# Kernel tuning notes

Measured on AMD Instinct MI355X. Metric: run time of the kernel, lower is better.

Reference implementation:

```python
import jax, jax.numpy as jnp
import numpy as np

N, K, DIM = 65536, 32, 64


def setup_inputs() -> dict:
    key = jax.random.key(0)
    k1, k2, k3, k4 = jax.random.split(key, 4)
    x = jax.random.normal(k1, (N, DIM), jnp.float32)
    log_pi = jax.random.normal(k2, (K, 1), jnp.float32)
    mu = jax.random.normal(k3, (K, DIM), jnp.float32)
    log_sigma_ = jax.random.normal(k4, (K, DIM, DIM), jnp.float32) / 100.0
    return {"x": x, "log_pi": log_pi, "mu": mu, "log_sigma_": log_sigma_}


def reference(x, log_pi, mu, log_sigma_):
    k, d = mu.shape
    # Faithful to torch: softmax over the size-1 last axis of (K,1) -> all ones.
    pi = jax.nn.softmax(log_pi, axis=-1)  # (K, 1)
    # scale_tril construction: strict lower triangle kept, diagonal -> exp(diag) + 1e-3
    diag = jnp.exp(jnp.diagonal(log_sigma_, axis1=-2, axis2=-1)) + 1e-3  # (K, d)
    L = jnp.tril(log_sigma_, -1) + jnp.eye(d, dtype=x.dtype) * diag[:, None, :]  # (K, d, d)
    # batched MVN log_prob via triangular solve
    diff = x[:, None, :] - mu[None, :, :]            # (N, K, d)
    b = jnp.transpose(diff, (1, 2, 0))               # (K, d, N)
    z = jax.scipy.linalg.solve_triangular(L, b, lower=True)  # (K, d, N)
    maha = jnp.sum(z * z, axis=1)                    # (K, N)
    logdet = jnp.sum(jnp.log(diag), axis=-1)         # (K,)
    logp = -0.5 * (maha + d * jnp.log(2.0 * jnp.pi)) - logdet[:, None]  # (K, N)
    p = jnp.exp(logp).T                              # (N, K)
    return jnp.log(jnp.matmul(p, pi).squeeze())      # (N,)
```

## Files before the change

kernel.cpp:

```cpp
#include <hip/hip_runtime.h>

#define KK 32
#define DD 64
#define NB 65536
#define PAD 68
#define FRAGS 6
#define SLOT (FRAGS * 64)
#define MREF 103.0f
#define L2E 1.4426950408889634f

typedef __attribute__((ext_vector_type(8))) short bf16x8;
typedef __attribute__((ext_vector_type(4))) float f32x4;
typedef __attribute__((ext_vector_type(16))) float f32x16;

__device__ inline short f2bf(float f) {
  uint32_t u = __builtin_bit_cast(uint32_t, f);
  uint32_t r = (u + 0x7fffu + ((u >> 16) & 1u)) >> 16;
  return (short)(r & 0xffffu);
}
__device__ inline uint4 pack8(const short* v) {
  uint4 u;
  u.x = (uint32_t)(unsigned short)v[0] | ((uint32_t)(unsigned short)v[1] << 16);
  u.y = (uint32_t)(unsigned short)v[2] | ((uint32_t)(unsigned short)v[3] << 16);
  u.z = (uint32_t)(unsigned short)v[4] | ((uint32_t)(unsigned short)v[5] << 16);
  u.w = (uint32_t)(unsigned short)v[6] | ((uint32_t)(unsigned short)v[7] << 16);
  return u;
}

__device__ __forceinline__ void gl_lds16(const uint4* g, uint4* l) {
  __builtin_amdgcn_global_load_lds(
      (__attribute__((address_space(1))) void*)g,
      (__attribute__((address_space(3))) void*)l, 16, 0, 0);
}

__global__ __launch_bounds__(256) void md_prep(const float* __restrict__ ls,
                                               const float* __restrict__ mu,
                                               uint4* __restrict__ Bp,
                                               float* __restrict__ Cc,
                                               float* __restrict__ Kcl2) {
  __shared__ float Ls[DD * DD];
  __shared__ float Ys[DD * PAD];
  __shared__ float invdL[DD];
  __shared__ float muL[DD];
  const int k = blockIdx.x, t = threadIdx.x;
  const int j = t >> 2, sub = t & 3;
  const float* __restrict__ lsk = ls + (size_t)k * DD * DD;

#pragma unroll
  for (int it = 0; it < 4; ++it) {
    const int o = (it * 256 + t) * 4;
    *(float4*)&Ls[o] = *(const float4*)&lsk[o];
  }
  if (t < DD) muL[t] = mu[k * DD + t];
  __syncthreads();
  if (t < DD) invdL[t] = 1.0f / (expf(Ls[t * DD + t]) + 1e-3f);
  __syncthreads();

  const float invdj = invdL[j];
  float z[16];
#pragma unroll
  for (int mi = 0; mi < 16; ++mi) z[mi] = 0.f;
#pragma unroll
  for (int i = 0; i < DD; ++i) {
    float p = 0.f;
#pragma unroll
    for (int mi = 0; mi < 16; ++mi) {
      if (4 * mi < i) {
        const int m = 4 * mi + sub;
        p = fmaf(Ls[i * DD + m], (m < i) ? z[mi] : 0.f, p);
      }
    }
    p += __shfl_xor(p, 1, 64);
    p += __shfl_xor(p, 2, 64);
    const float zi = (i == j) ? invdj : -p * invdL[i];
    if (sub == (i & 3)) z[i >> 2] = zi;
  }
#pragma unroll
  for (int mi = 0; mi < 16; ++mi) Ys[(4 * mi + sub) * PAD + j] = z[mi];
  __syncthreads();

  {
    float p = 0.f;
#pragma unroll
    for (int mi = 0; mi < 16; ++mi) {
      const int m = 4 * mi + sub;
      p = fmaf(Ys[j * PAD + m], muL[m], p);
    }
    p += __shfl_xor(p, 1, 64);
    p += __shfl_xor(p, 2, 64);
    if (sub == 0) Cc[k * DD + j] = p;
  }

  if (t < DD) {
    float r = -logf(invdL[t]);
#pragma unroll
    for (int off = 32; off > 0; off >>= 1) r += __shfl_down(r, off, 64);
    if (t == 0)
      Kcl2[k] = (MREF - 0.5f * (64.0f * 1.83787706640934534f) - r) * L2E;
  }

  if (t < DD) {
    const int r32 = t & 31, h = t >> 5;
    uint4* slot = Bp + (size_t)k * SLOT;
#pragma unroll
    for (int it = 0; it < 2; ++it) {
#pragma unroll
      for (int kt = 0; kt < 4; ++kt) {
        if (it == 0 && kt >= 2) continue;
        const int i = it * 32 + r32;
        short hh[8];
#pragma unroll
        for (int jj = 0; jj < 8; ++jj) {
          const int m = kt * 16 + h * 8 + jj;
          const float v = Ys[i * PAD + m] - ((i == m) ? 1.0f : 0.0f);
          hh[jj] = f2bf(v);
        }
        const int fi = (it == 0) ? kt : (2 + kt);
        slot[fi * 64 + t] = pack8(hh);
      }
    }
  }
}

__global__ __launch_bounds__(256, 2) void md_main(const float* __restrict__ x,
                                                  const uint4* __restrict__ Bp,
                                                  const float* __restrict__ Cc,
                                                  const float* __restrict__ Kcl2,
                                                  float* __restrict__ out) {
  __shared__ uint4 lds4[8 * SLOT];
  __shared__ float CcL[KK * DD];
  __shared__ float sOut[2 * 128];
  const int tid = threadIdx.x, lane = tid & 63, w = tid >> 6;
  const int sg = w & 1, kg = w >> 1;
  const int sblk = blockIdx.x;
  const int base = sblk * 128 + sg * 64;
  const int k0 = kg * 16;
  const int c32 = lane & 31, h = lane >> 5;

  bf16x8 Xb[2][4];
#pragma unroll
  for (int st = 0; st < 2; ++st) {
#pragma unroll
    for (int kt = 0; kt < 4; ++kt) {
      const float* src = x + (size_t)(base + st * 32 + c32) * DD + kt * 16 + h * 8;
      const float4 v0 = *(const float4*)src;
      const float4 v1 = *(const float4*)(src + 4);
      const float f[8] = {v0.x, v0.y, v0.z, v0.w, v1.x, v1.y, v1.z, v1.w};
      bf16x8 hb;
#pragma unroll
      for (int jj = 0; jj < 8; ++jj) hb[jj] = f2bf(f[jj]);
      Xb[st][kt] = hb;
    }
  }

  f32x16 xg[2][2];
#pragma unroll
  for (int it = 0; it < 2; ++it)
#pragma unroll
    for (int st = 0; st < 2; ++st)
#pragma unroll
      for (int g = 0; g < 4; ++g) {
        const f32x4 v = *(const f32x4*)&x[(size_t)(base + st * 32 + c32) * DD +
                                          it * 32 + g * 8 + 4 * h];
        xg[it][st][4 * g + 0] = v[0];
        xg[it][st][4 * g + 1] = v[1];
        xg[it][st][4 * g + 2] = v[2];
        xg[it][st][4 * g + 3] = v[3];
      }

#pragma unroll
  for (int it = 0; it < 8; ++it)
    CcL[it * 256 + tid] = Cc[it * 256 + tid];

  {
    const uint4* src = Bp + (size_t)(k0 + sg) * SLOT;
#pragma unroll
    for (int t = 0; t < 6; ++t)
      gl_lds16(src + t * 64 + lane,
               &lds4[((kg * 2 + 0) * 2 + sg) * SLOT + t * 64]);
  }
  __syncthreads();

  float run_s[2] = {0.f, 0.f};

#pragma unroll
  for (int kp = 0; kp < 8; ++kp) {
    const int p = kp & 1;
    if (kp < 7) {
      const uint4* src = Bp + (size_t)(k0 + 2 * (kp + 1) + sg) * SLOT;
#pragma unroll
      for (int t = 0; t < 6; ++t)
        gl_lds16(src + t * 64 + lane,
                 &lds4[((kg * 2 + (1 - p)) * 2 + sg) * SLOT + t * 64]);
    }

#pragma unroll
    for (int c = 0; c < 2; ++c) {
      const int kabs = k0 + 2 * kp + c;
      const float kc = Kcl2[kabs];
      const uint4* buf = &lds4[((kg * 2 + p) * 2 + c) * SLOT];

      f32x4 cv[2][4];
#pragma unroll
      for (int it = 0; it < 2; ++it)
#pragma unroll
        for (int g = 0; g < 4; ++g)
          cv[it][g] = *(const f32x4*)&CcL[kabs * DD + it * 32 + g * 8 + 4 * h];

      const bf16x8 A0 = *(const bf16x8*)&buf[0 * 64 + lane];
      const bf16x8 A1 = *(const bf16x8*)&buf[1 * 64 + lane];
      const bf16x8 A2 = *(const bf16x8*)&buf[2 * 64 + lane];
      const bf16x8 A3 = *(const bf16x8*)&buf[3 * 64 + lane];
      const bf16x8 A4 = *(const bf16x8*)&buf[4 * 64 + lane];
      const bf16x8 A5 = *(const bf16x8*)&buf[5 * 64 + lane];

#pragma unroll
      for (int st = 0; st < 2; ++st) {
        f32x16 acc;
#pragma unroll
        for (int it = 0; it < 2; ++it) {
          f32x16 z;
#pragma unroll
          for (int g = 0; g < 4; ++g) {
#pragma unroll
            for (int r = 0; r < 4; ++r)
              z[4 * g + r] = xg[it][st][4 * g + r] - cv[it][g][r];
          }
          if (it == 0) {
            z = __builtin_amdgcn_mfma_f32_32x32x16_bf16(A0, Xb[st][0], z, 0, 0, 0);
            z = __builtin_amdgcn_mfma_f32_32x32x16_bf16(A1, Xb[st][1], z, 0, 0, 0);
            acc = z * z;
          } else {
            z = __builtin_amdgcn_mfma_f32_32x32x16_bf16(A2, Xb[st][0], z, 0, 0, 0);
            z = __builtin_amdgcn_mfma_f32_32x32x16_bf16(A3, Xb[st][1], z, 0, 0, 0);
            z = __builtin_amdgcn_mfma_f32_32x32x16_bf16(A4, Xb[st][2], z, 0, 0, 0);
            z = __builtin_amdgcn_mfma_f32_32x32x16_bf16(A5, Xb[st][3], z, 0, 0, 0);
            acc += z * z;
          }
        }
        const float t0 = (acc[0] + acc[1]) + (acc[2] + acc[3]);
        const float t1 = (acc[4] + acc[5]) + (acc[6] + acc[7]);
        const float t2 = (acc[8] + acc[9]) + (acc[10] + acc[11]);
        const float t3 = (acc[12] + acc[13]) + (acc[14] + acc[15]);
        float s = (t0 + t1) + (t2 + t3);
        s += __shfl_xor(s, 32, 64);
        const float tt = fmaf(-0.5f * L2E, s, kc);
        run_s[st] += __builtin_amdgcn_exp2f(tt);
      }
    }

    if (kp < 7) __syncthreads();
  }

  if (h == 0) {
#pragma unroll
    for (int st = 0; st < 2; ++st)
      sOut[kg * 128 + sg * 64 + st * 32 + c32] = run_s[st];
  }
  __syncthreads();
  if (tid < 128) {
    const float S = sOut[tid] + sOut[128 + tid];
    out[sblk * 128 + tid] = logf(S) - MREF;
  }
}

extern "C" void kernel_launch(void* const* d_in, const int* in_sizes, int n_in,
                              void* d_out, int out_size, void* d_ws, size_t ws_size,
                              hipStream_t stream) {
  const float* x  = (const float*)d_in[0];
  const float* mu = (const float*)d_in[2];
  const float* ls = (const float*)d_in[3];
  float* out = (float*)d_out;

  char* ws = (char*)d_ws;
  uint4* Bp   = (uint4*)ws;
  float* Cc   = (float*)(ws + (size_t)KK * SLOT * 16);
  float* Kcl2 = Cc + KK * DD;

  md_prep<<<KK, 256, 0, stream>>>(ls, mu, Bp, Cc, Kcl2);
  md_main<<<NB / 128, 256, 0, stream>>>(x, Bp, Cc, Kcl2, out);
}
```

Measured before the change: 99.56 us.

## Load MFMA A-fragments directly from global memory instead of LDS double-buffer

Removes the async global-to-LDS double-buffered staging of per-component B fragments and the per-iteration block barriers. Each wave now reads its bf16 A operands straight from global/L2 for each of its 16 components. This frees LDS (possibly raising occupancy) and removes synchronization, at the cost of exposing global load latency before each MFMA chain, since nothing is prefetched.

Result: no change. 98.33 us (median of 2 runs) (-1.2%).

```diff
diff --git a/kernel.cpp b/kernel.cpp
--- a/kernel.cpp
+++ b/kernel.cpp
@@ -25,12 +25,6 @@
   u.z = (uint32_t)(unsigned short)v[4] | ((uint32_t)(unsigned short)v[5] << 16);
   u.w = (uint32_t)(unsigned short)v[6] | ((uint32_t)(unsigned short)v[7] << 16);
   return u;
-}
-
-__device__ __forceinline__ void gl_lds16(const uint4* g, uint4* l) {
-  __builtin_amdgcn_global_load_lds(
-      (__attribute__((address_space(1))) void*)g,
-      (__attribute__((address_space(3))) void*)l, 16, 0, 0);
 }
 
 __global__ __launch_bounds__(256) void md_prep(const float* __restrict__ ls,
@@ -127,7 +121,6 @@
                                                   const float* __restrict__ Cc,
                                                   const float* __restrict__ Kcl2,
                                                   float* __restrict__ out) {
-  __shared__ uint4 lds4[8 * SLOT];
   __shared__ float CcL[KK * DD];
   __shared__ float sOut[2 * 128];
   const int tid = threadIdx.x, lane = tid & 63, w = tid >> 6;
@@ -171,85 +164,63 @@
 #pragma unroll
   for (int it = 0; it < 8; ++it)
     CcL[it * 256 + tid] = Cc[it * 256 + tid];
-
-  {
-    const uint4* src = Bp + (size_t)(k0 + sg) * SLOT;
-#pragma unroll
-    for (int t = 0; t < 6; ++t)
-      gl_lds16(src + t * 64 + lane,
-               &lds4[((kg * 2 + 0) * 2 + sg) * SLOT + t * 64]);
-  }
   __syncthreads();
 
   float run_s[2] = {0.f, 0.f};
 
 #pragma unroll
-  for (int kp = 0; kp < 8; ++kp) {
-    const int p = kp & 1;
-    if (kp < 7) {
-      const uint4* src = Bp + (size_t)(k0 + 2 * (kp + 1) + sg) * SLOT;
-#pragma unroll
-      for (int t = 0; t < 6; ++t)
-        gl_lds16(src + t * 64 + lane,
-                 &lds4[((kg * 2 + (1 - p)) * 2 + sg) * SLOT + t * 64]);
-    }
-
-#pragma unroll
-    for (int c = 0; c < 2; ++c) {
-      const int kabs = k0 + 2 * kp + c;
-      const float kc = Kcl2[kabs];
-      const uint4* buf = &lds4[((kg * 2 + p) * 2 + c) * SLOT];
-
-      f32x4 cv[2][4];
-#pragma unroll
-      for (int it = 0; it < 2; ++it)
-#pragma unroll
-        for (int g = 0; g < 4; ++g)
-          cv[it][g] = *(const f32x4*)&CcL[kabs * DD + it * 32 + g * 8 + 4 * h];
-
-      const bf16x8 A0 = *(const bf16x8*)&buf[0 * 64 + lane];
-      const bf16x8 A1 = *(const bf16x8*)&buf[1 * 64 + lane];
-      const bf16x8 A2 = *(const bf16x8*)&buf[2 * 64 + lane];
-      const bf16x8 A3 = *(const bf16x8*)&buf[3 * 64 + lane];
-      const bf16x8 A4 = *(const bf16x8*)&buf[4 * 64 + lane];
-      const bf16x8 A5 = *(const bf16x8*)&buf[5 * 64 + lane];
-
-#pragma unroll
-      for (int st = 0; st < 2; ++st) {
-        f32x16 acc;
-#pragma unroll
-        for (int it = 0; it < 2; ++it) {
-          f32x16 z;
-#pragma unroll
-          for (int g = 0; g < 4; ++g) {
-#pragma unroll
-            for (int r = 0; r < 4; ++r)
-              z[4 * g + r] = xg[it][st][4 * g + r] - cv[it][g][r];
-          }
-          if (it == 0) {
-            z = __builtin_amdgcn_mfma_f32_32x32x16_bf16(A0, Xb[st][0], z, 0, 0, 0);
-            z = __builtin_amdgcn_mfma_f32_32x32x16_bf16(A1, Xb[st][1], z, 0, 0, 0);
-            acc = z * z;
-          } else {
-            z = __builtin_amdgcn_mfma_f32_32x32x16_bf16(A2, Xb[st][0], z, 0, 0, 0);
-            z = __builtin_amdgcn_mfma_f32_32x32x16_bf16(A3, Xb[st][1], z, 0, 0, 0);
-            z = __builtin_amdgcn_mfma_f32_32x32x16_bf16(A4, Xb[st][2], z, 0, 0, 0);
-            z = __builtin_amdgcn_mfma_f32_32x32x16_bf16(A5, Xb[st][3], z, 0, 0, 0);
-            acc += z * z;
-          }
+  for (int ci = 0; ci < 16; ++ci) {
+    const int kabs = k0 + ci;
+    const float kc = Kcl2[kabs];
+    const uint4* __restrict__ buf = Bp + (size_t)kabs * SLOT;
+
+    f32x4 cv[2][4];
+#pragma unroll
+    for (int it = 0; it < 2; ++it)
+#pragma unroll
+      for (int g = 0; g < 4; ++g)
+        cv[it][g] = *(const f32x4*)&CcL[kabs * DD + it * 32 + g * 8 + 4 * h];
+
+    const bf16x8 A0 = *(const bf16x8*)&buf[0 * 64 + lane];
+    const bf16x8 A1 = *(const bf16x8*)&buf[1 * 64 + lane];
+    const bf16x8 A2 = *(const bf16x8*)&buf[2 * 64 + lane];
+    const bf16x8 A3 = *(const bf16x8*)&buf[3 * 64 + lane];
+    const bf16x8 A4 = *(const bf16x8*)&buf[4 * 64 + lane];
+    const bf16x8 A5 = *(const bf16x8*)&buf[5 * 64 + lane];
+
+#pragma unroll
+    for (int st = 0; st < 2; ++st) {
+      f32x16 acc;
+#pragma unroll
+      for (int it = 0; it < 2; ++it) {
+        f32x16 z;
+#pragma unroll
+        for (int g = 0; g < 4; ++g) {
+#pragma unroll
+          for (int r = 0; r < 4; ++r)
+            z[4 * g + r] = xg[it][st][4 * g + r] - cv[it][g][r];
         }
-        const float t0 = (acc[0] + acc[1]) + (acc[2] + acc[3]);
-        const float t1 = (acc[4] + acc[5]) + (acc[6] + acc[7]);
-        const float t2 = (acc[8] + acc[9]) + (acc[10] + acc[11]);
-        const float t3 = (acc[12] + acc[13]) + (acc[14] + acc[15]);
-        float s = (t0 + t1) + (t2 + t3);
-        s += __shfl_xor(s, 32, 64);
-        const float tt = fmaf(-0.5f * L2E, s, kc);
-        run_s[st] += __builtin_amdgcn_exp2f(tt);
-      }
-    }
-
-    if (kp < 7) __syncthreads();
+        if (it == 0) {
+          z = __builtin_amdgcn_mfma_f32_32x32x16_bf16(A0, Xb[st][0], z, 0, 0, 0);
+          z = __builtin_amdgcn_mfma_f32_32x32x16_bf16(A1, Xb[st][1], z, 0, 0, 0);
+          acc = z * z;
+        } else {
+          z = __builtin_amdgcn_mfma_f32_32x32x16_bf16(A2, Xb[st][0], z, 0, 0, 0);
+          z = __builtin_amdgcn_mfma_f32_32x32x16_bf16(A3, Xb[st][1], z, 0, 0, 0);
+          z = __builtin_amdgcn_mfma_f32_32x32x16_bf16(A4, Xb[st][2], z, 0, 0, 0);
+          z = __builtin_amdgcn_mfma_f32_32x32x16_bf16(A5, Xb[st][3], z, 0, 0, 0);
+          acc += z * z;
+        }
+      }
+      const float t0 = (acc[0] + acc[1]) + (acc[2] + acc[3]);
+      const float t1 = (acc[4] + acc[5]) + (acc[6] + acc[7]);
+      const float t2 = (acc[8] + acc[9]) + (acc[10] + acc[11]);
+      const float t3 = (acc[12] + acc[13]) + (acc[14] + acc[15]);
+      float s = (t0 + t1) + (t2 + t3);
+      s += __shfl_xor(s, 32, 64);
+      const float tt = fmaf(-0.5f * L2E, s, kc);
+      run_s[st] += __builtin_amdgcn_exp2f(tt);
+    }
   }
 
   if (h == 0) {
```
